# Kernel optimization log

Hardware: AMD Instinct MI355X
Metric: run time of the kernel (lower is better)

Reference implementation:

```python
import jax, jax.numpy as jnp
import numpy as np

D_MODEL = 1024
NUM_HEADS = 16
D_K = D_MODEL // NUM_HEADS  # 64


def setup_inputs() -> dict:
    key = jax.random.key(0)
    ks = jax.random.split(key, 12)
    B, S = 4, 2048
    scale = 1.0 / np.sqrt(D_MODEL)
    inp = {
        'query': jax.random.normal(ks[0], (B, S, D_MODEL), jnp.float32),
        'key': jax.random.normal(ks[1], (B, S, D_MODEL), jnp.float32),
        'value': jax.random.normal(ks[2], (B, S, D_MODEL), jnp.float32),
        # per-head projection weights stacked along head axis [H, d_model, d_k]
        'Wq': jax.random.normal(ks[3], (NUM_HEADS, D_MODEL, D_K), jnp.float32) * scale,
        'bq': jax.random.normal(ks[4], (NUM_HEADS, D_K), jnp.float32) * 0.01,
        'Wk': jax.random.normal(ks[5], (NUM_HEADS, D_MODEL, D_K), jnp.float32) * scale,
        'bk': jax.random.normal(ks[6], (NUM_HEADS, D_K), jnp.float32) * 0.01,
        'Wv': jax.random.normal(ks[7], (NUM_HEADS, D_MODEL, D_K), jnp.float32) * scale,
        'bv': jax.random.normal(ks[8], (NUM_HEADS, D_K), jnp.float32) * 0.01,
        'Wo': jax.random.normal(ks[9], (NUM_HEADS * D_K, D_MODEL), jnp.float32) * scale,
        'bo': jax.random.normal(ks[10], (D_MODEL,), jnp.float32) * 0.01,
    }
    return inp


def reference(query, key, value, Wq, bq, Wk, bk, Wv, bv, Wo, bo):
    # Per-head linear projections, batched over heads: [B,S,D] x [H,D,K] -> [B,H,S,K]
    q = jnp.einsum('bsd,hdk->bhsk', query, Wq) + bq[None, :, None, :]
    k = jnp.einsum('bsd,hdk->bhsk', key, Wk) + bk[None, :, None, :]
    v = jnp.einsum('bsd,hdk->bhsk', value, Wv) + bv[None, :, None, :]
    # Scaled dot-product attention per head
    scores = jnp.einsum('bhqk,bhsk->bhqs', q, k) / jnp.sqrt(jnp.asarray(D_K, q.dtype))
    attn = jax.nn.softmax(scores, axis=-1)
    heads = jnp.einsum('bhqs,bhsk->bhqk', attn, v)  # [B,H,S,K]
    # Concat heads -> [B,S,H*K], then output projection
    B, H, S, K = heads.shape
    concat = jnp.transpose(heads, (0, 2, 1, 3)).reshape(B, S, H * K)
    return concat @ Wo + bo
```

## Files before the change

kernel.cpp:

```cpp
#include <hip/hip_runtime.h>
#include <hip/hip_bf16.h>

typedef __bf16 bf16_t;
typedef __bf16 bf16x8 __attribute__((ext_vector_type(8)));
typedef __bf16 bf16x4 __attribute__((ext_vector_type(4)));
typedef float f32x4 __attribute__((ext_vector_type(4)));
typedef float f32x16 __attribute__((ext_vector_type(16)));

constexpr int BB = 4;
constexpr int SS = 2048;
constexpr int DM = 1024;
constexpr int NH = 16;
constexpr int DK = 64;
constexpr int MROWS = BB * SS;

template <int N> struct IC { static constexpr int V = N; };

__device__ inline uint32_t pkbf16(float a, float b) {
    union { bf16_t h[2]; uint32_t u; } x;
    x.h[0] = (bf16_t)a; x.h[1] = (bf16_t)b;
    return x.u;
}

__device__ inline float fexp2(float x) { return __builtin_amdgcn_exp2f(x); }

__device__ inline void gld16(const bf16_t* g, bf16_t* l) {
    __builtin_amdgcn_global_load_lds((const __attribute__((address_space(1))) void*)g,
                                     (__attribute__((address_space(3))) void*)l, 16, 0, 0);
}

__device__ inline f32x16 mfma32(bf16x8 a, bf16x8 b, f32x16 c) {
    return __builtin_amdgcn_mfma_f32_32x32x16_bf16(a, b, c, 0, 0, 0);
}

__device__ inline bf16x8 lds_rd(const bf16_t* base, int row, int slot) {
    return *(const bf16x8*)((const char*)base + row * 128 + ((slot ^ (row & 7)) << 4));
}

__global__ __launch_bounds__(256) void k_transpose3(const float* __restrict__ s0,
                                                    const float* __restrict__ s1,
                                                    const float* __restrict__ s2,
                                                    bf16_t* __restrict__ dst) {
    __shared__ float tile[32][33];
    const int zz = blockIdx.z;
    const int zt = zz >> 4, zh = zz & 15;
    const float* src = (zt == 0) ? s0 : ((zt == 1) ? s1 : s2);
    const int cb = blockIdx.x * 32, rb = blockIdx.y * 32;
    const long zoff = (long)zh * DM * DK;
    bf16_t* d = dst + (size_t)zt * DM * DM + (size_t)zh * DK * DM;
    const int tx = threadIdx.x & 31, ty = threadIdx.x >> 5;
#pragma unroll
    for (int i = 0; i < 4; ++i) {
        int r = rb + ty + i * 8;
        tile[ty + i * 8][tx] = src[zoff + (long)r * DK + cb + tx];
    }
    __syncthreads();
#pragma unroll
    for (int i = 0; i < 4; ++i) {
        int c = cb + ty + i * 8;
        d[(long)c * DM + rb + tx] = (bf16_t)tile[tx][ty + i * 8];
    }
}

__global__ __launch_bounds__(256) void k_transpose(const float* __restrict__ src,
                                                   bf16_t* __restrict__ dst,
                                                   int R, int C) {
    __shared__ float tile[32][33];
    const int cb = blockIdx.x * 32, rb = blockIdx.y * 32;
    const int tx = threadIdx.x & 31, ty = threadIdx.x >> 5;
#pragma unroll
    for (int i = 0; i < 4; ++i) {
        int r = rb + ty + i * 8;
        tile[ty + i * 8][tx] = src[(long)r * C + cb + tx];
    }
    __syncthreads();
#pragma unroll
    for (int i = 0; i < 4; ++i) {
        int c = cb + ty + i * 8;
        dst[(long)c * R + rb + tx] = (bf16_t)tile[tx][ty + i * 8];
    }
}

__global__ __launch_bounds__(256) void k_proj(
    const float* __restrict__ Aq, const float* __restrict__ Ak, const float* __restrict__ Av,
    const bf16_t* __restrict__ Wt,
    const float* __restrict__ bq, const float* __restrict__ bk, const float* __restrict__ bv,
    bf16_t* __restrict__ qkv) {
    const int hwid = blockIdx.x;
    const int c = hwid & 7, j = hwid >> 3;
    const int z = j >> 6;
    const int r = j & 63;
    const int n0 = (r & 7) * 128;
    const int m0 = (c * 8 + (r >> 3)) * 128;

    const float* A = (z == 0) ? Aq : ((z == 1) ? Ak : Av);
    const float* bias = (z == 0) ? bq : ((z == 1) ? bk : bv);
    const float scale = (z == 0) ? (float)(1.4426950408889634 / 8.0) : 1.0f;
    const bf16_t* Bt = Wt + (size_t)z * DM * DM;
    bf16_t* outp = qkv + (size_t)z * BB * NH * SS * DK;

    __shared__ __align__(16) union SM {
        struct { bf16_t a[128][72]; bf16_t b[2][8192]; } s;
        bf16_t vt[128][136];
    } sm;

    const int t = threadIdx.x;
    const int lane = t & 63, w = t >> 6;
    const int lr = lane & 15, lg = lane >> 4;
    const int wr = w >> 1, wc = w & 1;

    f32x4 acc[4][4] = {};
    float4 apf[8];

    const int brow = t >> 3, bssl = t & 7;
    const size_t bsrc = (size_t)(n0 + brow) * DM + ((bssl ^ (brow & 7)) << 3);
    const int ar0 = t >> 4, aseg = t & 15;

#pragma unroll
    for (int p = 0; p < 4; ++p)
        gld16(&Bt[bsrc + p * 32 * DM], &sm.s.b[0][(p * 256 + w * 64) * 8]);
#pragma unroll
    for (int p = 0; p < 8; ++p)
        apf[p] = *(const float4*)&A[(size_t)(m0 + ar0 + p * 16) * DM + aseg * 4];
#pragma unroll
    for (int p = 0; p < 8; ++p) {
        bf16x4 pk = {(bf16_t)apf[p].x, (bf16_t)apf[p].y, (bf16_t)apf[p].z, (bf16_t)apf[p].w};
        *(bf16x4*)&sm.s.a[ar0 + p * 16][aseg * 4] = pk;
    }
    __syncthreads();

    auto body = [&](auto icur, int kt) {
        constexpr int cur = decltype(icur)::V;
        const int k1 = (kt + 1) * 64;
        if (kt + 1 < 16) {
#pragma unroll
            for (int p = 0; p < 4; ++p)
                gld16(&Bt[bsrc + k1 + p * 32 * DM], &sm.s.b[cur ^ 1][(p * 256 + w * 64) * 8]);
#pragma unroll
            for (int p = 0; p < 8; ++p)
                apf[p] = *(const float4*)&A[(size_t)(m0 + ar0 + p * 16) * DM + k1 + aseg * 4];
        }
#pragma unroll
        for (int ks = 0; ks < 2; ++ks) {
            const int lk = ks * 32 + lg * 8;
            bf16x8 af[4], bfm[4];
#pragma unroll
            for (int i = 0; i < 4; ++i) af[i] = *(const bf16x8*)&sm.s.a[wr * 64 + i * 16 + lr][lk];
#pragma unroll
            for (int jj = 0; jj < 4; ++jj) bfm[jj] = lds_rd(sm.s.b[cur], wc * 64 + jj * 16 + lr, ks * 4 + lg);
#pragma unroll
            for (int i = 0; i < 4; ++i)
#pragma unroll
                for (int jj = 0; jj < 4; ++jj)
                    acc[i][jj] = __builtin_amdgcn_mfma_f32_16x16x32_bf16(af[i], bfm[jj], acc[i][jj], 0, 0, 0);
        }
        __syncthreads();
        if (kt + 1 < 16) {
#pragma unroll
            for (int p = 0; p < 8; ++p) {
                bf16x4 pk = {(bf16_t)apf[p].x, (bf16_t)apf[p].y, (bf16_t)apf[p].z, (bf16_t)apf[p].w};
                *(bf16x4*)&sm.s.a[ar0 + p * 16][aseg * 4] = pk;
            }
        }
        __syncthreads();
    };

#pragma unroll 1
    for (int kt = 0; kt < 16; kt += 2) {
        body(IC<0>{}, kt);
        body(IC<1>{}, kt + 1);
    }

    const int b = m0 >> 11, s0 = m0 & (SS - 1);
    if (z == 2) {
#pragma unroll
        for (int i = 0; i < 4; ++i)
#pragma unroll
            for (int jj = 0; jj < 4; ++jj) {
                int col = wc * 64 + jj * 16 + lr;
                float bv_ = bias[n0 + col];
#pragma unroll
                for (int rr = 0; rr < 4; ++rr)
                    sm.vt[col][wr * 64 + i * 16 + lg * 4 + rr] = (bf16_t)(acc[i][jj][rr] + bv_);
            }
        __syncthreads();
#pragma unroll
        for (int pp = 0; pp < 8; ++pp) {
            int d = pp * 16 + (t >> 4);
            int cs = (t & 15) * 8;
            bf16x8 v = *(const bf16x8*)&sm.vt[d][cs];
            int h = (n0 + d) >> 6, dd = d & 63;
            *(bf16x8*)&outp[((size_t)(b * NH + h) * DK + dd) * SS + s0 + cs] = v;
        }
    } else {
#pragma unroll
        for (int i = 0; i < 4; ++i) {
#pragma unroll
            for (int jj = 0; jj < 4; ++jj) {
                int col = wc * 64 + jj * 16 + lr;
                int h = (n0 + col) >> 6, ko = col & 63;
                float bv_ = bias[n0 + col];
#pragma unroll
                for (int rr = 0; rr < 4; ++rr) {
                    int s = s0 + wr * 64 + i * 16 + lg * 4 + rr;
                    float v = (acc[i][jj][rr] + bv_) * scale;
                    outp[(((size_t)b * NH + h) * SS + s) * DK + ko] = (bf16_t)v;
                }
            }
        }
    }
}

__global__ __launch_bounds__(256, 4) void k_attn(const bf16_t* __restrict__ qkv,
                                                 bf16_t* __restrict__ concat) {
    const int hw = blockIdx.x + 16 * (blockIdx.y + 16 * blockIdx.z);
    const int lb = (hw & 7) * 128 + (hw >> 3);
    const int qt = lb & 15;
    const int h = (lb >> 4) & 15;
    const int b = lb >> 8;

    const size_t PH = (size_t)BB * NH * SS * DK;
    const bf16_t* qp = qkv + ((size_t)(b * NH + h) * SS) * DK;
    const bf16_t* kp = qp + PH;
    const bf16_t* vtp = qkv + 2 * PH + (size_t)(b * NH + h) * DK * SS;

    __shared__ __align__(16) bf16_t k_lds[2][4096];
    __shared__ __align__(16) bf16_t v_lds[2][4096];

    const int t = threadIdx.x;
    const int lane = t & 63, w = t >> 6;
    const int l31 = lane & 31;
    const bool hf = (lane >> 5) != 0;

    const int sr = t >> 3, ssl = t & 7;
    const int prow = (sr & ~12) | ((sr & 4) << 1) | ((sr & 8) >> 1);
    const int ssw = (ssl ^ (sr & 7)) * 8;
    const size_t okA = (size_t)prow * DK + ssw;
    const size_t ovA = (size_t)sr * SS + ssw;

    const int qbase = qt * 128 + w * 32;
    bf16x8 qf[4];
#pragma unroll
    for (int ks = 0; ks < 4; ++ks)
        qf[ks] = *(const bf16x8*)&qp[(size_t)(qbase + l31) * DK + ks * 16 + (hf ? 8 : 0)];

    f32x16 oacc0 = {}, oacc1 = {};
    float lsum = 0.f;
    f32x16 zc = {};
    asm volatile("" : "+v"(zc));

    constexpr int NT = SS / 64;

    gld16(kp + okA, &k_lds[0][w * 512]);
    gld16(kp + okA + 32 * DK, &k_lds[0][w * 512 + 2048]);
    gld16(vtp + ovA, &v_lds[0][w * 512]);
    gld16(vtp + ovA + (size_t)32 * SS, &v_lds[0][w * 512 + 2048]);
    __syncthreads();

    const bf16_t* kpp = kp + okA + 4096;
    const bf16_t* vpp = vtp + ovA + 64;

    auto body = [&](auto icur, int it) {
        constexpr int cur = decltype(icur)::V;
        if (it + 1 < NT) {
            gld16(kpp, &k_lds[cur ^ 1][w * 512]);
            gld16(kpp + 32 * DK, &k_lds[cur ^ 1][w * 512 + 2048]);
            gld16(vpp, &v_lds[cur ^ 1][w * 512]);
            gld16(vpp + (size_t)32 * SS, &v_lds[cur ^ 1][w * 512 + 2048]);
            kpp += 4096;
            vpp += 64;
        }
        f32x16 sc0, sc1;
        __builtin_amdgcn_s_setprio(1);
        {
            bf16x8 kf0 = lds_rd(k_lds[cur], l31, hf);
            bf16x8 kf1 = lds_rd(k_lds[cur], 32 + l31, hf);
            sc0 = mfma32(kf0, qf[0], zc);
            sc1 = mfma32(kf1, qf[0], zc);
        }
#pragma unroll
        for (int ks = 1; ks < 4; ++ks) {
            bf16x8 kf0 = lds_rd(k_lds[cur], l31, 2 * ks + hf);
            bf16x8 kf1 = lds_rd(k_lds[cur], 32 + l31, 2 * ks + hf);
            sc0 = mfma32(kf0, qf[ks], sc0);
            sc1 = mfma32(kf1, qf[ks], sc1);
        }
        auto pvstep = [&](auto ikq, const f32x16& s, auto ibase) {
            constexpr int kq = decltype(ikq)::V;
            constexpr int base = decltype(ibase)::V;
            float p[8];
#pragma unroll
            for (int i = 0; i < 8; ++i) p[i] = fexp2(s[base + i]);
            lsum += ((p[0] + p[1]) + (p[2] + p[3])) + ((p[4] + p[5]) + (p[6] + p[7]));
            union { uint32_t u[4]; bf16x8 v; } pb;
#pragma unroll
            for (int i = 0; i < 4; ++i) pb.u[i] = pkbf16(p[2 * i], p[2 * i + 1]);
            bf16x8 vf0 = lds_rd(v_lds[cur], l31, 2 * kq + hf);
            bf16x8 vf1 = lds_rd(v_lds[cur], 32 + l31, 2 * kq + hf);
            oacc0 = mfma32(vf0, pb.v, oacc0);
            oacc1 = mfma32(vf1, pb.v, oacc1);
        };
        pvstep(IC<0>{}, sc0, IC<0>{});
        pvstep(IC<1>{}, sc0, IC<8>{});
        pvstep(IC<2>{}, sc1, IC<0>{});
        pvstep(IC<3>{}, sc1, IC<8>{});
        __builtin_amdgcn_s_setprio(0);
        __syncthreads();
    };

#pragma unroll 1
    for (int t2 = 0; t2 < NT; t2 += 2) {
        body(IC<0>{}, t2);
        body(IC<1>{}, t2 + 1);
    }

    float l = lsum + __shfl_xor(lsum, 32);
    float inv = 1.0f / l;
    const int q = qbase + l31;
#pragma unroll
    for (int dt = 0; dt < 2; ++dt) {
#pragma unroll
        for (int quad = 0; quad < 4; ++quad) {
            const f32x16& oa = dt ? oacc1 : oacc0;
            bf16x4 ov = {(bf16_t)(oa[quad * 4 + 0] * inv),
                         (bf16_t)(oa[quad * 4 + 1] * inv),
                         (bf16_t)(oa[quad * 4 + 2] * inv),
                         (bf16_t)(oa[quad * 4 + 3] * inv)};
            int col = dt * 32 + quad * 8 + (hf ? 4 : 0);
            *(bf16x4*)&concat[((size_t)b * SS + q) * DM + h * 64 + col] = ov;
        }
    }
}

__global__ __launch_bounds__(256) void k_out(const bf16_t* __restrict__ Ab,
                                             const bf16_t* __restrict__ Wot,
                                             const float* __restrict__ bo,
                                             float* __restrict__ out) {
    const int hwid = blockIdx.x;
    const int c = hwid & 7, j = hwid >> 3;
    const int n0 = (j & 7) * 128;
    const int m0 = (c * 8 + (j >> 3)) * 128;

    __shared__ __align__(16) bf16_t a_lds[128 * 64];
    __shared__ __align__(16) bf16_t b_lds[128 * 64];

    const int t = threadIdx.x;
    const int lane = t & 63, w = t >> 6;
    const int lr = lane & 15, lg = lane >> 4;
    const int wr = w >> 1, wc = w & 1;

    f32x4 acc[4][4] = {};

    for (int kt = 0; kt < 16; ++kt) {
        const int k0 = kt * 64;
#pragma unroll
        for (int p = 0; p < 4; ++p) {
            int id = p * 256 + t;
            int row = id >> 3, ssl = id & 7;
            int sc = (ssl ^ (row & 7)) << 3;
            gld16(&Ab[(size_t)(m0 + row) * DM + k0 + sc], a_lds + (size_t)(p * 256 + w * 64) * 8);
            gld16(&Wot[(size_t)(n0 + row) * DM + k0 + sc], b_lds + (size_t)(p * 256 + w * 64) * 8);
        }
        __syncthreads();
#pragma unroll
        for (int ks = 0; ks < 2; ++ks) {
            bf16x8 af[4], bfm[4];
#pragma unroll
            for (int i = 0; i < 4; ++i) af[i] = lds_rd(a_lds, wr * 64 + i * 16 + lr, ks * 4 + lg);
#pragma unroll
            for (int jj = 0; jj < 4; ++jj) bfm[jj] = lds_rd(b_lds, wc * 64 + jj * 16 + lr, ks * 4 + lg);
#pragma unroll
            for (int i = 0; i < 4; ++i)
#pragma unroll
                for (int jj = 0; jj < 4; ++jj)
                    acc[i][jj] = __builtin_amdgcn_mfma_f32_16x16x32_bf16(af[i], bfm[jj], acc[i][jj], 0, 0, 0);
        }
        __syncthreads();
    }
#pragma unroll
    for (int i = 0; i < 4; ++i) {
#pragma unroll
        for (int jj = 0; jj < 4; ++jj) {
            int col = n0 + wc * 64 + jj * 16 + lr;
            float bv_ = bo[col];
#pragma unroll
            for (int rr = 0; rr < 4; ++rr) {
                int mrow = m0 + wr * 64 + i * 16 + lg * 4 + rr;
                out[(size_t)mrow * DM + col] = acc[i][jj][rr] + bv_;
            }
        }
    }
}

extern "C" void kernel_launch(void* const* d_in, const int* in_sizes, int n_in,
                              void* d_out, int out_size, void* d_ws, size_t ws_size,
                              hipStream_t stream) {
    const float* query = (const float*)d_in[0];
    const float* key   = (const float*)d_in[1];
    const float* value = (const float*)d_in[2];
    const float* Wq = (const float*)d_in[3];
    const float* bq = (const float*)d_in[4];
    const float* Wk = (const float*)d_in[5];
    const float* bk = (const float*)d_in[6];
    const float* Wv = (const float*)d_in[7];
    const float* bv = (const float*)d_in[8];
    const float* Wo = (const float*)d_in[9];
    const float* bo = (const float*)d_in[10];

    char* ws = (char*)d_ws;
    bf16_t* qkv    = (bf16_t*)ws;
    bf16_t* Wt     = (bf16_t*)(ws + (size_t)50331648);
    bf16_t* Wot    = (bf16_t*)(ws + (size_t)50331648 + 6291456);
    bf16_t* concat = (bf16_t*)(ws + (size_t)50331648 + 8388608);

    k_transpose3<<<dim3(2, 32, 48), 256, 0, stream>>>(Wq, Wk, Wv, Wt);
    k_transpose<<<dim3(32, 32, 1), 256, 0, stream>>>(Wo, Wot, DM, DM);

    k_proj<<<dim3(1536), 256, 0, stream>>>(query, key, value, Wt, bq, bk, bv, qkv);
    k_attn<<<dim3(16, 16, 4), 256, 0, stream>>>(qkv, concat);
    k_out<<<dim3(512), 256, 0, stream>>>(concat, Wot, bo, (float*)d_out);
}
```

Baseline: 196.1 us.

## Pre-convert activations to bf16 and load both GEMM operands via direct-to-LDS loads

Adds a separate kernel that converts query/key/value from fp32 to bf16 into workspace. The projection GEMM then loads both A and B tiles with global_load_lds into swizzled LDS, with no register staging or in-loop conversion. It also drops the double-buffered prefetch pipeline in favour of a single buffer with load-sync-compute-sync. This adds an extra full pass over the activations (read 96MB fp32, write 48MB bf16) and loses load/compute overlap, in exchange for halving the bytes the GEMM reads and simplifying its inner loop. The concat buffer aliases the bf16 activation buffer, which is safe because the projection finishes before attention writes concat.

```diff
diff --git a/kernel.cpp b/kernel.cpp
--- a/kernel.cpp
+++ b/kernel.cpp
@@ -35,6 +35,21 @@
 
 __device__ inline bf16x8 lds_rd(const bf16_t* base, int row, int slot) {
     return *(const bf16x8*)((const char*)base + row * 128 + ((slot ^ (row & 7)) << 4));
+}
+
+__global__ __launch_bounds__(256) void k_cvtA(const float* __restrict__ Aq,
+                                              const float* __restrict__ Ak,
+                                              const float* __restrict__ Av,
+                                              bf16_t* __restrict__ dst) {
+    const size_t g = (size_t)blockIdx.x * 256 + threadIdx.x;
+    const size_t zi = g >> 20;
+    const size_t off = (g & 1048575) * 8;
+    const float* src = (zi == 0) ? Aq : ((zi == 1) ? Ak : Av);
+    float4 a = *(const float4*)&src[off];
+    float4 b = *(const float4*)&src[off + 4];
+    bf16x8 o = {(bf16_t)a.x, (bf16_t)a.y, (bf16_t)a.z, (bf16_t)a.w,
+                (bf16_t)b.x, (bf16_t)b.y, (bf16_t)b.z, (bf16_t)b.w};
+    *(bf16x8*)&dst[g * 8] = o;
 }
 
 __global__ __launch_bounds__(256) void k_transpose3(const float* __restrict__ s0,
@@ -82,8 +97,7 @@
 }
 
 __global__ __launch_bounds__(256) void k_proj(
-    const float* __restrict__ Aq, const float* __restrict__ Ak, const float* __restrict__ Av,
-    const bf16_t* __restrict__ Wt,
+    const bf16_t* __restrict__ Ab3, const bf16_t* __restrict__ Wt,
     const float* __restrict__ bq, const float* __restrict__ bk, const float* __restrict__ bv,
     bf16_t* __restrict__ qkv) {
     const int hwid = blockIdx.x;
@@ -93,14 +107,14 @@
     const int n0 = (r & 7) * 128;
     const int m0 = (c * 8 + (r >> 3)) * 128;
 
-    const float* A = (z == 0) ? Aq : ((z == 1) ? Ak : Av);
+    const bf16_t* A = Ab3 + (size_t)z * MROWS * DM;
     const float* bias = (z == 0) ? bq : ((z == 1) ? bk : bv);
     const float scale = (z == 0) ? (float)(1.4426950408889634 / 8.0) : 1.0f;
     const bf16_t* Bt = Wt + (size_t)z * DM * DM;
     bf16_t* outp = qkv + (size_t)z * BB * NH * SS * DK;
 
     __shared__ __align__(16) union SM {
-        struct { bf16_t a[128][72]; bf16_t b[2][8192]; } s;
+        struct { bf16_t a[128 * 64]; bf16_t b[128 * 64]; } s;
         bf16_t vt[128][136];
     } sm;
 
@@ -110,44 +124,31 @@
     const int wr = w >> 1, wc = w & 1;
 
     f32x4 acc[4][4] = {};
-    float4 apf[8];
-
-    const int brow = t >> 3, bssl = t & 7;
-    const size_t bsrc = (size_t)(n0 + brow) * DM + ((bssl ^ (brow & 7)) << 3);
-    const int ar0 = t >> 4, aseg = t & 15;
-
-#pragma unroll
-    for (int p = 0; p < 4; ++p)
-        gld16(&Bt[bsrc + p * 32 * DM], &sm.s.b[0][(p * 256 + w * 64) * 8]);
-#pragma unroll
-    for (int p = 0; p < 8; ++p)
-        apf[p] = *(const float4*)&A[(size_t)(m0 + ar0 + p * 16) * DM + aseg * 4];
-#pragma unroll
-    for (int p = 0; p < 8; ++p) {
-        bf16x4 pk = {(bf16_t)apf[p].x, (bf16_t)apf[p].y, (bf16_t)apf[p].z, (bf16_t)apf[p].w};
-        *(bf16x4*)&sm.s.a[ar0 + p * 16][aseg * 4] = pk;
-    }
-    __syncthreads();
-
-    auto body = [&](auto icur, int kt) {
-        constexpr int cur = decltype(icur)::V;
-        const int k1 = (kt + 1) * 64;
-        if (kt + 1 < 16) {
-#pragma unroll
-            for (int p = 0; p < 4; ++p)
-                gld16(&Bt[bsrc + k1 + p * 32 * DM], &sm.s.b[cur ^ 1][(p * 256 + w * 64) * 8]);
-#pragma unroll
-            for (int p = 0; p < 8; ++p)
-                apf[p] = *(const float4*)&A[(size_t)(m0 + ar0 + p * 16) * DM + k1 + aseg * 4];
-        }
+
+    const int row = t >> 3, ssl = t & 7;
+    const int scol = (ssl ^ (row & 7)) << 3;
+    const size_t asrc = (size_t)(m0 + row) * DM + scol;
+    const size_t bsrc = (size_t)(n0 + row) * DM + scol;
+    bf16_t* adst = &sm.s.a[0] + (size_t)t * 8 * 4;
+
+    for (int kt = 0; kt < 16; ++kt) {
+        const int k0 = kt * 64;
+#pragma unroll
+        for (int p = 0; p < 4; ++p) {
+            int id = p * 256 + t;
+            int rw = id >> 3, sl = id & 7;
+            int sc = (sl ^ (rw & 7)) << 3;
+            gld16(&A[(size_t)(m0 + rw) * DM + k0 + sc], sm.s.a + (size_t)(p * 256 + w * 64) * 8);
+            gld16(&Bt[(size_t)(n0 + rw) * DM + k0 + sc], sm.s.b + (size_t)(p * 256 + w * 64) * 8);
+        }
+        __syncthreads();
 #pragma unroll
         for (int ks = 0; ks < 2; ++ks) {
-            const int lk = ks * 32 + lg * 8;
             bf16x8 af[4], bfm[4];
 #pragma unroll
-            for (int i = 0; i < 4; ++i) af[i] = *(const bf16x8*)&sm.s.a[wr * 64 + i * 16 + lr][lk];
-#pragma unroll
-            for (int jj = 0; jj < 4; ++jj) bfm[jj] = lds_rd(sm.s.b[cur], wc * 64 + jj * 16 + lr, ks * 4 + lg);
+            for (int i = 0; i < 4; ++i) af[i] = lds_rd(sm.s.a, wr * 64 + i * 16 + lr, ks * 4 + lg);
+#pragma unroll
+            for (int jj = 0; jj < 4; ++jj) bfm[jj] = lds_rd(sm.s.b, wc * 64 + jj * 16 + lr, ks * 4 + lg);
 #pragma unroll
             for (int i = 0; i < 4; ++i)
 #pragma unroll
@@ -155,22 +156,7 @@
                     acc[i][jj] = __builtin_amdgcn_mfma_f32_16x16x32_bf16(af[i], bfm[jj], acc[i][jj], 0, 0, 0);
         }
         __syncthreads();
-        if (kt + 1 < 16) {
-#pragma unroll
-            for (int p = 0; p < 8; ++p) {
-                bf16x4 pk = {(bf16_t)apf[p].x, (bf16_t)apf[p].y, (bf16_t)apf[p].z, (bf16_t)apf[p].w};
-                *(bf16x4*)&sm.s.a[ar0 + p * 16][aseg * 4] = pk;
-            }
-        }
-        __syncthreads();
-    };
-
-#pragma unroll 1
-    for (int kt = 0; kt < 16; kt += 2) {
-        body(IC<0>{}, kt);
-        body(IC<1>{}, kt + 1);
-    }
-
+    }
     const int b = m0 >> 11, s0 = m0 & (SS - 1);
     if (z == 2) {
 #pragma unroll
@@ -410,13 +396,15 @@
     char* ws = (char*)d_ws;
     bf16_t* qkv    = (bf16_t*)ws;
     bf16_t* Wt     = (bf16_t*)(ws + (size_t)50331648);
-    bf16_t* Wot    = (bf16_t*)(ws + (size_t)50331648 + 6291456);
-    bf16_t* concat = (bf16_t*)(ws + (size_t)50331648 + 8388608);
-
+    bf16_t* Wot    = (bf16_t*)(ws + (size_t)56623104);
+    bf16_t* Ab     = (bf16_t*)(ws + (size_t)58720256);
+    bf16_t* concat = (bf16_t*)(ws + (size_t)58720256);
+
+    k_cvtA<<<dim3(12288), 256, 0, stream>>>(query, key, value, Ab);
     k_transpose3<<<dim3(2, 32, 48), 256, 0, stream>>>(Wq, Wk, Wv, Wt);
     k_transpose<<<dim3(32, 32, 1), 256, 0, stream>>>(Wo, Wot, DM, DM);
 
-    k_proj<<<dim3(1536), 256, 0, stream>>>(query, key, value, Wt, bq, bk, bv, qkv);
+    k_proj<<<dim3(1536), 256, 0, stream>>>(Ab, Wt, bq, bk, bv, qkv);
     k_attn<<<dim3(16, 16, 4), 256, 0, stream>>>(qkv, concat);
     k_out<<<dim3(512), 256, 0, stream>>>(concat, Wot, bo, (float*)d_out);
 }
```

After: 207.3 us. +5.7%, slower.
